# Kernel tuning notes

Hardware: AMD Instinct MI355X
Metric: run time of the kernel (lower is better)

Reference implementation:

```python
import jax, jax.numpy as jnp
import numpy as np

N_HEAD = 12
D_HEAD = 64


def setup_inputs() -> dict:
    key = jax.random.key(0)
    ks = jax.random.split(key, 9)
    bs, seq, d_model = 4, 2048, 768
    sc = 1.0 / np.sqrt(d_model)
    return {
        "q": jax.random.normal(ks[0], (bs, seq, d_model), jnp.float32),
        "k": jax.random.normal(ks[1], (bs, seq, d_model), jnp.float32),
        "v": jax.random.normal(ks[2], (bs, seq, d_model), jnp.float32),
        "Wq": jax.random.normal(ks[3], (d_model, d_model), jnp.float32) * sc,
        "bq": jax.random.normal(ks[4], (d_model,), jnp.float32) * 0.01,
        "Wk": jax.random.normal(ks[5], (d_model, d_model), jnp.float32) * sc,
        "bk": jax.random.normal(ks[6], (d_model,), jnp.float32) * 0.01,
        "Wv": jax.random.normal(ks[7], (d_model, d_model), jnp.float32) * sc,
        "bv": jax.random.normal(ks[8], (d_model,), jnp.float32) * 0.01,
    }


def _split_heads(x):
    # [bs, seq, n_head*d_head] -> [bs, n_head, seq, d_head]
    bs, seq, _ = x.shape
    return x.reshape(bs, seq, N_HEAD, D_HEAD).transpose(0, 2, 1, 3)


def reference(q, k, v, Wq, bq, Wk, bk, Wv, bv):
    # Linear projections (torch Linear: x @ W.T + b)
    wq = _split_heads(q @ Wq.T + bq)
    wk = _split_heads(k @ Wk.T + bk)
    wv = _split_heads(v @ Wv.T + bv)
    # scale=False in defaults -> raw dot products, no mask, dropout is eval no-op
    scores = jnp.einsum("bhqd,bhkd->bhqk", wq, wk)  # [bs, h, S, S]
    probs = jax.nn.softmax(scores, axis=-1)
    attn_vec = jnp.einsum("bhqk,bhkd->bhqd", probs, wv)
    bs, _, seq, _ = attn_vec.shape
    # merge heads -> [bs, seq, n_head*d_head]
    return attn_vec.transpose(0, 2, 1, 3).reshape(bs, seq, N_HEAD * D_HEAD)
```

## Files before the change

kernel.cpp:

```cpp
#include <hip/hip_runtime.h>
#include <stdint.h>

typedef _Float16 half8  __attribute__((ext_vector_type(8)));
typedef _Float16 half4v __attribute__((ext_vector_type(4)));
typedef float    floatx4 __attribute__((ext_vector_type(4)));

#define LOG2E 1.44269504088896340736f

__device__ __forceinline__ void gl_lds16(const _Float16* g, _Float16* l) {
  __builtin_amdgcn_global_load_lds(
      (__attribute__((address_space(1))) void*)g,
      (__attribute__((address_space(3))) void*)l, 16, 0, 0);
}

__device__ __forceinline__ float exp2_fast(float x) {
  float r;
  asm volatile("v_exp_f32 %0, %1\n\ts_nop 1" : "=v"(r) : "v"(x));
  return r;
}

struct CvtArgs {
  const float* src[6];
  _Float16*    dst[6];
  int          n[6];
};

__global__ void cvt_kernel(CvtArgs a) {
  const int z = blockIdx.y;
  const int n = a.n[z];
  const int i = (blockIdx.x * 256 + threadIdx.x) * 8;
  if (i >= n) return;
  const float4* s = (const float4*)(a.src[z] + i);
  float4 v0 = s[0], v1 = s[1];
  half8 h = { (_Float16)v0.x, (_Float16)v0.y, (_Float16)v0.z, (_Float16)v0.w,
              (_Float16)v1.x, (_Float16)v1.y, (_Float16)v1.z, (_Float16)v1.w };
  *(half8*)(a.dst[z] + i) = h;
}

__global__ __launch_bounds__(256, 2) void qkv_gemm(
    const _Float16* __restrict__ xh, const _Float16* __restrict__ wh,
    const float* __restrict__ bqp, const float* __restrict__ bkp, const float* __restrict__ bvp,
    _Float16* __restrict__ oq, _Float16* __restrict__ ok, _Float16* __restrict__ ovt)
{
  __shared__ __attribute__((aligned(16))) _Float16 As[128 * 32];
  __shared__ __attribute__((aligned(16))) _Float16 Bs[128 * 32];
  const int z  = blockIdx.z;
  const _Float16* X = xh + (size_t)z * 8192 * 768;
  const _Float16* W = wh + (size_t)z * 768 * 768;
  const int m0 = blockIdx.x * 128, n0 = blockIdx.y * 128;
  const int tid  = threadIdx.x;
  const int lane = tid & 63, wid = tid >> 6;
  const int wr = wid >> 1, wc = wid & 1;
  const int qd = lane >> 4, col = lane & 15;

  const floatx4 z4 = {0.f, 0.f, 0.f, 0.f};
  floatx4 acc[4][4];
  #pragma unroll
  for (int i = 0; i < 4; ++i)
    #pragma unroll
    for (int j = 0; j < 4; ++j) acc[i][j] = z4;

  const int c0 = tid, c1 = 256 + tid;
  const int ar0 = c0 >> 2, ac0 = (c0 & 3) * 8;
  const int ar1 = c1 >> 2, ac1 = (c1 & 3) * 8;

  for (int k0 = 0; k0 < 768; k0 += 32) {
    __syncthreads();
    gl_lds16(X + (size_t)(m0 + ar0) * 768 + k0 + ac0, As + c0 * 8);
    gl_lds16(X + (size_t)(m0 + ar1) * 768 + k0 + ac1, As + c1 * 8);
    gl_lds16(W + (size_t)(n0 + ar0) * 768 + k0 + ac0, Bs + c0 * 8);
    gl_lds16(W + (size_t)(n0 + ar1) * 768 + k0 + ac1, Bs + c1 * 8);
    __syncthreads();
    half8 af[4], bf[4];
    #pragma unroll
    for (int t = 0; t < 4; ++t)
      af[t] = *(const half8*)(As + (wr * 64 + t * 16 + col) * 32 + qd * 8);
    #pragma unroll
    for (int t = 0; t < 4; ++t)
      bf[t] = *(const half8*)(Bs + (wc * 64 + t * 16 + col) * 32 + qd * 8);
    #pragma unroll
    for (int i = 0; i < 4; ++i)
      #pragma unroll
      for (int j = 0; j < 4; ++j)
        acc[i][j] = __builtin_amdgcn_mfma_f32_16x16x32_f16(af[i], bf[j], acc[i][j], 0, 0, 0);
  }

  const float* bias = (z == 0) ? bqp : ((z == 1) ? bkp : bvp);
  if (z == 2) {
    #pragma unroll
    for (int j = 0; j < 4; ++j) {
      int n = n0 + wc * 64 + j * 16 + col;
      float bb = bias[n];
      #pragma unroll
      for (int i = 0; i < 4; ++i) {
        int m = m0 + wr * 64 + i * 16 + qd * 4;
        int b = m >> 11, s = m & 2047;
        half4v h;
        #pragma unroll
        for (int r = 0; r < 4; ++r) h[r] = (_Float16)(acc[i][j][r] + bb);
        *(half4v*)(ovt + ((size_t)(b * 768 + n)) * 2048 + s) = h;
      }
    }
  } else {
    _Float16* O = (z == 0) ? oq : ok;
    const float scale = (z == 0) ? LOG2E : 1.0f;
    #pragma unroll
    for (int j = 0; j < 4; ++j) {
      int n = n0 + wc * 64 + j * 16 + col;
      float bb = bias[n];
      int hh = n >> 6, d = n & 63;
      #pragma unroll
      for (int i = 0; i < 4; ++i) {
        int m = m0 + wr * 64 + i * 16 + qd * 4;
        int b = m >> 11, s = m & 2047;
        _Float16* p = O + (size_t)(b * 12 + hh) * 131072 + (size_t)s * 64 + d;
        #pragma unroll
        for (int r = 0; r < 4; ++r) p[(size_t)r * 64] = (_Float16)((acc[i][j][r] + bb) * scale);
      }
    }
  }
}

__global__ __launch_bounds__(256, 2) void attn_kernel(
    const _Float16* __restrict__ Qm,
    const _Float16* __restrict__ Km,
    const _Float16* __restrict__ Vt,
    float* __restrict__ out)
{
  __shared__ __attribute__((aligned(16))) _Float16 Qs[128 * 64];
  __shared__ __attribute__((aligned(16))) _Float16 Ks[128 * 64];
  __shared__ __attribute__((aligned(16))) _Float16 Vs[64 * 128];
  const int bh = blockIdx.y;
  const int q0 = blockIdx.x * 128;
  const int tid = threadIdx.x, lane = tid & 63, w = tid >> 6;
  const int qd = lane >> 4, col = lane & 15;
  const _Float16* Qg = Qm + (size_t)bh * 131072;
  const _Float16* Kg = Km + (size_t)bh * 131072;
  const _Float16* Vg = Vt + (size_t)bh * 131072;

  #pragma unroll
  for (int i = 0; i < 4; ++i) {
    int cc = i * 256 + tid, row = cc >> 3, pc = cc & 7;
    gl_lds16(Qg + (size_t)(q0 + row) * 64 + ((pc ^ (row & 7)) * 8), Qs + cc * 8);
  }
  __syncthreads();
  half8 qf[2][2];
  #pragma unroll
  for (int qt = 0; qt < 2; ++qt)
    #pragma unroll
    for (int ks = 0; ks < 2; ++ks) {
      int row = w * 32 + qt * 16 + col;
      qf[qt][ks] = *(const half8*)(Qs + row * 64 + (((ks * 4 + qd) ^ (row & 7)) * 8));
    }
  _Float16* Pb = Qs + w * 2048;

  float m2[2]   = {-INFINITY, -INFINITY};
  float lsum[2] = {0.f, 0.f};
  const floatx4 z4 = {0.f, 0.f, 0.f, 0.f};
  floatx4 o[4][2];
  #pragma unroll
  for (int dt = 0; dt < 4; ++dt)
    #pragma unroll
    for (int qt = 0; qt < 2; ++qt) o[dt][qt] = z4;

  for (int j0 = 0; j0 < 2048; j0 += 128) {
    __syncthreads();
    #pragma unroll
    for (int i = 0; i < 4; ++i) {
      int cc = i * 256 + tid, row = cc >> 3, pc = cc & 7;
      gl_lds16(Kg + (size_t)(j0 + row) * 64 + ((pc ^ (row & 7)) * 8), Ks + cc * 8);
    }
    #pragma unroll
    for (int i = 0; i < 4; ++i) {
      int cc = i * 256 + tid, row = cc >> 4, pc = cc & 15;
      gl_lds16(Vg + (size_t)row * 2048 + j0 + ((pc ^ (row & 15)) * 8), Vs + cc * 8);
    }
    __syncthreads();

    floatx4 st[8][2];
    #pragma unroll
    for (int t = 0; t < 8; ++t)
      #pragma unroll
      for (int qt = 0; qt < 2; ++qt) st[t][qt] = z4;
    #pragma unroll
    for (int t = 0; t < 8; ++t) {
      int row = t * 16 + col;
      #pragma unroll
      for (int ks = 0; ks < 2; ++ks) {
        half8 kf = *(const half8*)(Ks + row * 64 + (((ks * 4 + qd) ^ (row & 7)) * 8));
        #pragma unroll
        for (int qt = 0; qt < 2; ++qt)
          st[t][qt] = __builtin_amdgcn_mfma_f32_16x16x32_f16(kf, qf[qt][ks], st[t][qt], 0, 0, 0);
      }
    }

    #pragma unroll
    for (int qt = 0; qt < 2; ++qt) {
      float mx = -INFINITY;
      #pragma unroll
      for (int t = 0; t < 8; ++t) {
        floatx4 s = st[t][qt];
        mx = fmaxf(mx, fmaxf(fmaxf(s[0], s[1]), fmaxf(s[2], s[3])));
      }
      mx = fmaxf(mx, __shfl_xor(mx, 16, 64));
      mx = fmaxf(mx, __shfl_xor(mx, 32, 64));
      float mo = m2[qt];
      float mn = fmaxf(mo, mx);
      m2[qt] = mn;
      float alpha = exp2_fast(mo - mn);
      float rs = 0.f;
      #pragma unroll
      for (int t = 0; t < 8; ++t) {
        floatx4 s = st[t][qt];
        s[0] = exp2_fast(s[0] - mn);
        s[1] = exp2_fast(s[1] - mn);
        s[2] = exp2_fast(s[2] - mn);
        s[3] = exp2_fast(s[3] - mn);
        rs += (s[0] + s[1]) + (s[2] + s[3]);
        st[t][qt] = s;
      }
      rs += __shfl_xor(rs, 16, 64);
      rs += __shfl_xor(rs, 32, 64);
      lsum[qt] = lsum[qt] * alpha + rs;
      #pragma unroll
      for (int dt = 0; dt < 4; ++dt) {
        o[dt][qt][0] *= alpha; o[dt][qt][1] *= alpha;
        o[dt][qt][2] *= alpha; o[dt][qt][3] *= alpha;
      }
    }

    #pragma unroll
    for (int c = 0; c < 4; ++c) {
      #pragma unroll
      for (int tt = 0; tt < 2; ++tt) {
        int t = 2 * c + tt;
        #pragma unroll
        for (int qt = 0; qt < 2; ++qt) {
          int qq = qt * 16 + col;
          floatx4 s = st[t][qt];
          half4v p4 = {(_Float16)s[0], (_Float16)s[1], (_Float16)s[2], (_Float16)s[3]};
          *(half4v*)(Pb + qq * 40 + tt * 16 + qd * 4) = p4;
        }
      }
      half8 vf[4];
      #pragma unroll
      for (int dt = 0; dt < 4; ++dt) {
        int row = dt * 16 + col;
        vf[dt] = *(const half8*)(Vs + row * 128 + (((c * 4 + qd) ^ (row & 15)) * 8));
      }
      #pragma unroll
      for (int qt = 0; qt < 2; ++qt) {
        int qq = qt * 16 + col;
        half8 pf = *(const half8*)(Pb + qq * 40 + qd * 8);
        #pragma unroll
        for (int dt = 0; dt < 4; ++dt)
          o[dt][qt] = __builtin_amdgcn_mfma_f32_16x16x32_f16(vf[dt], pf, o[dt][qt], 0, 0, 0);
      }
    }
  }

  const int b = bh / 12, h = bh % 12;
  #pragma unroll
  for (int qt = 0; qt < 2; ++qt) {
    float inv = 1.0f / lsum[qt];
    int qg = q0 + w * 32 + qt * 16 + col;
    float* obase = out + ((size_t)b * 2048 + qg) * 768 + h * 64;
    #pragma unroll
    for (int dt = 0; dt < 4; ++dt) {
      floatx4 v = o[dt][qt];
      v[0] *= inv; v[1] *= inv; v[2] *= inv; v[3] *= inv;
      *(floatx4*)(obase + dt * 16 + qd * 4) = v;
    }
  }
}

extern "C" void kernel_launch(void* const* d_in, const int* in_sizes, int n_in,
                              void* d_out, int out_size, void* d_ws, size_t ws_size,
                              hipStream_t stream) {
  const float* q  = (const float*)d_in[0];
  const float* k  = (const float*)d_in[1];
  const float* v  = (const float*)d_in[2];
  const float* Wq = (const float*)d_in[3];
  const float* bq = (const float*)d_in[4];
  const float* Wk = (const float*)d_in[5];
  const float* bk = (const float*)d_in[6];
  const float* Wv = (const float*)d_in[7];
  const float* bv = (const float*)d_in[8];

  const size_t NX = 6291456;
  const size_t NW = 589824;
  const size_t need = (3 * NX + 3 * NW + 3 * NX) * sizeof(_Float16);
  if (ws_size < need) return;

  _Float16* xh = (_Float16*)d_ws;
  _Float16* wh = xh + 3 * NX;
  _Float16* qh = wh + 3 * NW;
  _Float16* kh = qh + NX;
  _Float16* vt = kh + NX;

  CvtArgs ca;
  ca.src[0] = q;  ca.src[1] = k;  ca.src[2] = v;
  ca.src[3] = Wq; ca.src[4] = Wk; ca.src[5] = Wv;
  ca.dst[0] = xh;          ca.dst[1] = xh + NX;     ca.dst[2] = xh + 2 * NX;
  ca.dst[3] = wh;          ca.dst[4] = wh + NW;     ca.dst[5] = wh + 2 * NW;
  ca.n[0] = (int)NX; ca.n[1] = (int)NX; ca.n[2] = (int)NX;
  ca.n[3] = (int)NW; ca.n[4] = (int)NW; ca.n[5] = (int)NW;

  cvt_kernel<<<dim3(3072, 6), 256, 0, stream>>>(ca);
  qkv_gemm<<<dim3(64, 6, 3), 256, 0, stream>>>(xh, wh, bq, bk, bv, qh, kh, vt);
  attn_kernel<<<dim3(16, 48), 256, 0, stream>>>(qh, kh, vt, (float*)d_out);
}
```

Baseline: 276.3 us.

## Double-buffer K/V tiles, keep P in registers, skip unneeded rescales

Shrinks the attention KV tile to 64 keys and double-buffers K and V in LDS, so the next tile's async global-to-LDS copy overlaps the current tile's compute. It also drops one of the two barriers per tile. P now stays in registers, fed directly to 16x16x16 MFMAs instead of going through an LDS write and reload, and Q is read straight from global memory. The output rescale by alpha is skipped when no row max in the wavefront changed, and launch bounds now request 3 blocks per CU. In exchange there are more loop iterations with smaller MFMA K-depth, plus tighter register pressure at the higher occupancy target.

```diff
diff --git a/kernel.cpp b/kernel.cpp
--- a/kernel.cpp
+++ b/kernel.cpp
@@ -11,12 +11,6 @@
   __builtin_amdgcn_global_load_lds(
       (__attribute__((address_space(1))) void*)g,
       (__attribute__((address_space(3))) void*)l, 16, 0, 0);
-}
-
-__device__ __forceinline__ float exp2_fast(float x) {
-  float r;
-  asm volatile("v_exp_f32 %0, %1\n\ts_nop 1" : "=v"(r) : "v"(x));
-  return r;
 }
 
 struct CvtArgs {
@@ -121,41 +115,145 @@
   }
 }
 
-__global__ __launch_bounds__(256, 2) void attn_kernel(
+
+__device__ __forceinline__ void stage_kv(const _Float16* __restrict__ Kg,
+                                         const _Float16* __restrict__ Vg,
+                                         _Float16* ksd, _Float16* vsd, int j0, int tid) {
+  #pragma unroll
+  for (int i = 0; i < 2; ++i) {
+    int c = i * 256 + tid;
+    int row = c >> 3, sc = c & 7;
+    gl_lds16(Kg + (size_t)(j0 + row) * 64 + ((sc ^ (row & 7)) * 8), ksd + c * 8);
+    gl_lds16(Vg + (size_t)row * 2048 + j0 + ((sc ^ (row & 7)) * 8), vsd + c * 8);
+  }
+}
+
+template <int BUF>
+__device__ __forceinline__ void attn_body(
+    int jnext, const _Float16* __restrict__ Kg, const _Float16* __restrict__ Vg,
+    _Float16* Ks, _Float16* Vs, int tid,
+    const half8 (&qf)[2][2], int kb0, int kb1, const int (&vb)[4],
+    float (&m)[2], float (&l)[2], floatx4 (&o)[4][2])
+{
+  if (jnext < 2048)
+    stage_kv(Kg, Vg, Ks + (1 - BUF) * 4096, Vs + (1 - BUF) * 4096, jnext, tid);
+
+  const char* ksb = (const char*)Ks;
+  const char* vsb = (const char*)Vs;
+  const floatx4 z4 = {0.f, 0.f, 0.f, 0.f};
+
+  floatx4 st[4][2];
+  #pragma unroll
+  for (int t = 0; t < 4; ++t) {
+    half8 kf0 = *(const half8*)(ksb + BUF * 8192 + t * 2048 + kb0);
+    half8 kf1 = *(const half8*)(ksb + BUF * 8192 + t * 2048 + kb1);
+    #pragma unroll
+    for (int qt = 0; qt < 2; ++qt) {
+      st[t][qt] = __builtin_amdgcn_mfma_f32_16x16x32_f16(kf0, qf[qt][0], z4, 0, 0, 0);
+      st[t][qt] = __builtin_amdgcn_mfma_f32_16x16x32_f16(kf1, qf[qt][1], st[t][qt], 0, 0, 0);
+    }
+  }
+
+  float mn[2], rs[2];
+  half4v pf[4][2];
+  #pragma unroll
+  for (int qt = 0; qt < 2; ++qt) {
+    float mx = fmaxf(
+        fmaxf(fmaxf(fmaxf(st[0][qt][0], st[0][qt][1]), fmaxf(st[0][qt][2], st[0][qt][3])),
+              fmaxf(fmaxf(st[1][qt][0], st[1][qt][1]), fmaxf(st[1][qt][2], st[1][qt][3]))),
+        fmaxf(fmaxf(fmaxf(st[2][qt][0], st[2][qt][1]), fmaxf(st[2][qt][2], st[2][qt][3])),
+              fmaxf(fmaxf(st[3][qt][0], st[3][qt][1]), fmaxf(st[3][qt][2], st[3][qt][3]))));
+    mx = fmaxf(mx, __shfl_xor(mx, 16, 64));
+    mx = fmaxf(mx, __shfl_xor(mx, 32, 64));
+    mn[qt] = fmaxf(m[qt], mx);
+  }
+  bool upd = (mn[0] > m[0]) || (mn[1] > m[1]);
+
+  #pragma unroll
+  for (int qt = 0; qt < 2; ++qt) {
+    float r = 0.f;
+    #pragma unroll
+    for (int t = 0; t < 4; ++t) {
+      float e0 = __builtin_amdgcn_exp2f(st[t][qt][0] - mn[qt]);
+      float e1 = __builtin_amdgcn_exp2f(st[t][qt][1] - mn[qt]);
+      float e2 = __builtin_amdgcn_exp2f(st[t][qt][2] - mn[qt]);
+      float e3 = __builtin_amdgcn_exp2f(st[t][qt][3] - mn[qt]);
+      auto lo = __builtin_amdgcn_cvt_pkrtz(e0, e1);
+      auto hi = __builtin_amdgcn_cvt_pkrtz(e2, e3);
+      half4v p = {static_cast<_Float16>(lo[0]), static_cast<_Float16>(lo[1]),
+                  static_cast<_Float16>(hi[0]), static_cast<_Float16>(hi[1])};
+      pf[t][qt] = p;
+      r += (e0 + e1) + (e2 + e3);
+    }
+    r += __shfl_xor(r, 16, 64);
+    r += __shfl_xor(r, 32, 64);
+    rs[qt] = r;
+  }
+
+  if (__any(upd)) {
+    #pragma unroll
+    for (int qt = 0; qt < 2; ++qt) {
+      float alpha = __builtin_amdgcn_exp2f(m[qt] - mn[qt]);
+      m[qt] = mn[qt];
+      l[qt] = l[qt] * alpha + rs[qt];
+      #pragma unroll
+      for (int dt = 0; dt < 4; ++dt) {
+        o[dt][qt][0] *= alpha; o[dt][qt][1] *= alpha;
+        o[dt][qt][2] *= alpha; o[dt][qt][3] *= alpha;
+      }
+    }
+  } else {
+    l[0] += rs[0];
+    l[1] += rs[1];
+  }
+
+  #pragma unroll
+  for (int dt = 0; dt < 4; ++dt) {
+    #pragma unroll
+    for (int t = 0; t < 4; ++t) {
+      half4v vf = *(const half4v*)(vsb + BUF * 8192 + dt * 2048 + vb[t]);
+      #pragma unroll
+      for (int qt = 0; qt < 2; ++qt)
+        o[dt][qt] = __builtin_amdgcn_mfma_f32_16x16x16f16(vf, pf[t][qt], o[dt][qt], 0, 0, 0);
+    }
+  }
+  __syncthreads();
+}
+
+__global__ __launch_bounds__(256, 3) void attn_kernel(
     const _Float16* __restrict__ Qm,
     const _Float16* __restrict__ Km,
     const _Float16* __restrict__ Vt,
     float* __restrict__ out)
 {
-  __shared__ __attribute__((aligned(16))) _Float16 Qs[128 * 64];
-  __shared__ __attribute__((aligned(16))) _Float16 Ks[128 * 64];
-  __shared__ __attribute__((aligned(16))) _Float16 Vs[64 * 128];
+  __shared__ __attribute__((aligned(16))) _Float16 Ks[2 * 4096];
+  __shared__ __attribute__((aligned(16))) _Float16 Vs[2 * 4096];
   const int bh = blockIdx.y;
   const int q0 = blockIdx.x * 128;
   const int tid = threadIdx.x, lane = tid & 63, w = tid >> 6;
-  const int qd = lane >> 4, col = lane & 15;
+  const int qd = lane >> 4, col = lane & 15, c7 = col & 7;
   const _Float16* Qg = Qm + (size_t)bh * 131072;
   const _Float16* Kg = Km + (size_t)bh * 131072;
   const _Float16* Vg = Vt + (size_t)bh * 131072;
 
-  #pragma unroll
-  for (int i = 0; i < 4; ++i) {
-    int cc = i * 256 + tid, row = cc >> 3, pc = cc & 7;
-    gl_lds16(Qg + (size_t)(q0 + row) * 64 + ((pc ^ (row & 7)) * 8), Qs + cc * 8);
-  }
-  __syncthreads();
   half8 qf[2][2];
   #pragma unroll
   for (int qt = 0; qt < 2; ++qt)
     #pragma unroll
-    for (int ks = 0; ks < 2; ++ks) {
-      int row = w * 32 + qt * 16 + col;
-      qf[qt][ks] = *(const half8*)(Qs + row * 64 + (((ks * 4 + qd) ^ (row & 7)) * 8));
-    }
-  _Float16* Pb = Qs + w * 2048;
-
-  float m2[2]   = {-INFINITY, -INFINITY};
-  float lsum[2] = {0.f, 0.f};
+    for (int ks = 0; ks < 2; ++ks)
+      qf[qt][ks] = *(const half8*)(Qg + (size_t)(q0 + w * 32 + qt * 16 + col) * 64
+                                   + (ks * 4 + qd) * 8);
+
+  const int kb0 = col * 128 + ((qd ^ c7) * 16);
+  const int kb1 = col * 128 + (((4 + qd) ^ c7) * 16);
+  const int vq = (qd >> 1) ^ c7;
+  int vb[4];
+  #pragma unroll
+  for (int t = 0; t < 4; ++t)
+    vb[t] = col * 128 + (qd & 1) * 8 + ((vq ^ (2 * t)) * 16);
+
+  float m[2] = {-1e30f, -1e30f};
+  float l[2] = {0.f, 0.f};
   const floatx4 z4 = {0.f, 0.f, 0.f, 0.f};
   floatx4 o[4][2];
   #pragma unroll
@@ -163,106 +261,18 @@
     #pragma unroll
     for (int qt = 0; qt < 2; ++qt) o[dt][qt] = z4;
 
-  for (int j0 = 0; j0 < 2048; j0 += 128) {
-    __syncthreads();
-    #pragma unroll
-    for (int i = 0; i < 4; ++i) {
-      int cc = i * 256 + tid, row = cc >> 3, pc = cc & 7;
-      gl_lds16(Kg + (size_t)(j0 + row) * 64 + ((pc ^ (row & 7)) * 8), Ks + cc * 8);
-    }
-    #pragma unroll
-    for (int i = 0; i < 4; ++i) {
-      int cc = i * 256 + tid, row = cc >> 4, pc = cc & 15;
-      gl_lds16(Vg + (size_t)row * 2048 + j0 + ((pc ^ (row & 15)) * 8), Vs + cc * 8);
-    }
-    __syncthreads();
-
-    floatx4 st[8][2];
-    #pragma unroll
-    for (int t = 0; t < 8; ++t)
-      #pragma unroll
-      for (int qt = 0; qt < 2; ++qt) st[t][qt] = z4;
-    #pragma unroll
-    for (int t = 0; t < 8; ++t) {
-      int row = t * 16 + col;
-      #pragma unroll
-      for (int ks = 0; ks < 2; ++ks) {
-        half8 kf = *(const half8*)(Ks + row * 64 + (((ks * 4 + qd) ^ (row & 7)) * 8));
-        #pragma unroll
-        for (int qt = 0; qt < 2; ++qt)
-          st[t][qt] = __builtin_amdgcn_mfma_f32_16x16x32_f16(kf, qf[qt][ks], st[t][qt], 0, 0, 0);
-      }
-    }
-
-    #pragma unroll
-    for (int qt = 0; qt < 2; ++qt) {
-      float mx = -INFINITY;
-      #pragma unroll
-      for (int t = 0; t < 8; ++t) {
-        floatx4 s = st[t][qt];
-        mx = fmaxf(mx, fmaxf(fmaxf(s[0], s[1]), fmaxf(s[2], s[3])));
-      }
-      mx = fmaxf(mx, __shfl_xor(mx, 16, 64));
-      mx = fmaxf(mx, __shfl_xor(mx, 32, 64));
-      float mo = m2[qt];
-      float mn = fmaxf(mo, mx);
-      m2[qt] = mn;
-      float alpha = exp2_fast(mo - mn);
-      float rs = 0.f;
-      #pragma unroll
-      for (int t = 0; t < 8; ++t) {
-        floatx4 s = st[t][qt];
-        s[0] = exp2_fast(s[0] - mn);
-        s[1] = exp2_fast(s[1] - mn);
-        s[2] = exp2_fast(s[2] - mn);
-        s[3] = exp2_fast(s[3] - mn);
-        rs += (s[0] + s[1]) + (s[2] + s[3]);
-        st[t][qt] = s;
-      }
-      rs += __shfl_xor(rs, 16, 64);
-      rs += __shfl_xor(rs, 32, 64);
-      lsum[qt] = lsum[qt] * alpha + rs;
-      #pragma unroll
-      for (int dt = 0; dt < 4; ++dt) {
-        o[dt][qt][0] *= alpha; o[dt][qt][1] *= alpha;
-        o[dt][qt][2] *= alpha; o[dt][qt][3] *= alpha;
-      }
-    }
-
-    #pragma unroll
-    for (int c = 0; c < 4; ++c) {
-      #pragma unroll
-      for (int tt = 0; tt < 2; ++tt) {
-        int t = 2 * c + tt;
-        #pragma unroll
-        for (int qt = 0; qt < 2; ++qt) {
-          int qq = qt * 16 + col;
-          floatx4 s = st[t][qt];
-          half4v p4 = {(_Float16)s[0], (_Float16)s[1], (_Float16)s[2], (_Float16)s[3]};
-          *(half4v*)(Pb + qq * 40 + tt * 16 + qd * 4) = p4;
-        }
-      }
-      half8 vf[4];
-      #pragma unroll
-      for (int dt = 0; dt < 4; ++dt) {
-        int row = dt * 16 + col;
-        vf[dt] = *(const half8*)(Vs + row * 128 + (((c * 4 + qd) ^ (row & 15)) * 8));
-      }
-      #pragma unroll
-      for (int qt = 0; qt < 2; ++qt) {
-        int qq = qt * 16 + col;
-        half8 pf = *(const half8*)(Pb + qq * 40 + qd * 8);
-        #pragma unroll
-        for (int dt = 0; dt < 4; ++dt)
-          o[dt][qt] = __builtin_amdgcn_mfma_f32_16x16x32_f16(vf[dt], pf, o[dt][qt], 0, 0, 0);
-      }
-    }
+  stage_kv(Kg, Vg, Ks, Vs, 0, tid);
+  __syncthreads();
+
+  for (int jj = 0; jj < 2048; jj += 128) {
+    attn_body<0>(jj + 64,  Kg, Vg, Ks, Vs, tid, qf, kb0, kb1, vb, m, l, o);
+    attn_body<1>(jj + 128, Kg, Vg, Ks, Vs, tid, qf, kb0, kb1, vb, m, l, o);
   }
 
   const int b = bh / 12, h = bh % 12;
   #pragma unroll
   for (int qt = 0; qt < 2; ++qt) {
-    float inv = 1.0f / lsum[qt];
+    float inv = 1.0f / l[qt];
     int qg = q0 + w * 32 + qt * 16 + col;
     float* obase = out + ((size_t)b * 2048 + qg) * 768 + h * 64;
     #pragma unroll
```

New measurement: 255.7 us. 1.08x faster.
